# Optimization experiments

Measured on AMD Instinct MI355X. Metric: run time of the kernel, lower is better.

## Reference

```python
import jax, jax.numpy as jnp
import numpy as np

N = 50000      # nodes
F = 256        # num_features
H = 128        # hidden_size
R = 16         # num_relations
E = 800000     # edges
C = 7          # num_classes
NB = 30        # num_bases (hard-coded in module)


def setup_inputs() -> dict:
    key = jax.random.key(0)
    ks = jax.random.split(key, 16)
    g = lambda k, shape, fan_in: jax.random.normal(k, shape, jnp.float32) / np.float32(np.sqrt(fan_in))
    inp = {
        "x": jax.random.normal(ks[0], (N, F), jnp.float32),
        "edge_index": jax.random.randint(ks[1], (2, E), 0, N),
        "edge_norm": jax.random.uniform(ks[2], (E,), jnp.float32),
        "edge_type": jax.random.randint(ks[3], (E,), 0, R),
        "seq_lengths": jax.random.randint(ks[4], (16,), 1, 100),
        "umask": jnp.ones((16, 110), jnp.float32),
        "nodal_attn": 0,
        "avec": 0,
        # RGCNConv (basis decomposition)
        "basis": g(ks[5], (NB, F, H), F),
        "comp": g(ks[6], (R, NB), NB),
        "root1": g(ks[7], (F, H), F),
        "bias1": jnp.zeros((H,), jnp.float32),
        # GraphConv
        "w_rel": g(ks[8], (H, H), H),
        "w_root": g(ks[9], (H, H), H),
        "bias2": jnp.zeros((H,), jnp.float32),
        # classification head
        "lin_w": g(ks[10], (F + H, H), F + H),
        "lin_b": jnp.zeros((H,), jnp.float32),
        "fc_w": g(ks[11], (H, C), H),
        "fc_b": jnp.zeros((C,), jnp.float32),
    }
    return inp


def reference(x, edge_index, edge_norm, edge_type, seq_lengths, umask,
              nodal_attn, avec, basis, comp, root1, bias1,
              w_rel, w_root, bias2, lin_w, lin_b, fc_w, fc_b):
    src, dst = edge_index[0], edge_index[1]

    # ---- RGCNConv: basis-decomposed relational conv, mean aggr per relation ----
    W = jnp.einsum('rb,bio->rio', comp, basis)          # [R,F,H]
    xW = jnp.einsum('ni,rio->nro', x, W)                # [N,R,H]
    msgs = xW[src, edge_type]                           # [E,H]
    seg = dst * R + edge_type                           # (dst, relation) segment id
    cnt = jax.ops.segment_sum(jnp.ones((E,), jnp.float32), seg, num_segments=N * R)
    inv = 1.0 / jnp.maximum(cnt, 1.0)
    agg1 = jax.ops.segment_sum(msgs * inv[seg][:, None], dst, num_segments=N)
    out1 = agg1 + x @ root1 + bias1                     # [N,H]

    # ---- GraphConv: sum aggr + root transform ----
    agg2 = jax.ops.segment_sum(out1[src], dst, num_segments=N)  # [N,H]
    out2 = agg2 @ w_rel + bias2 + out1 @ w_root         # [N,H]

    # ---- classification head (nodal_attn=False path; dropout is identity in eval) ----
    emotions = jnp.concatenate([x, out2], axis=-1)      # [N,F+H]
    hidden = jax.nn.relu(emotions @ lin_w + lin_b)      # [N,H]
    logits = hidden @ fc_w + fc_b                       # [N,C]
    return jax.nn.log_softmax(logits, axis=1)
```

## Files before the change

kernel.cpp:

```cpp
#include <hip/hip_runtime.h>
#include <hip/hip_bf16.h>
#include <stdint.h>

#define NN 50000
#define FF 256
#define HH 128
#define RR 16
#define EE 800000
#define CC 7
#define NB_ 30

typedef __attribute__((ext_vector_type(8))) short short8;
typedef __attribute__((ext_vector_type(4))) float f32x4;

__device__ __forceinline__ float bf2f(unsigned short u){
  union { unsigned int i; float f; } x; x.i = ((unsigned int)u) << 16; return x.f;
}
__device__ __forceinline__ unsigned short f2bf(float f){
  union { unsigned int i; float f; } x; x.f = f;
  unsigned int r = x.i + 0x7fffu + ((x.i >> 16) & 1u);
  return (unsigned short)(r >> 16);
}

__device__ __forceinline__ void gld16(const unsigned short* g, unsigned short* l){
  __builtin_amdgcn_global_load_lds(
      (const __attribute__((address_space(1))) unsigned int*)g,
      (__attribute__((address_space(3))) unsigned int*)l, 16, 0, 0);
}

template<bool BIAS, bool RELU, bool RASTER>
__global__ __launch_bounds__(256) void gemm_bt(
    const unsigned short* __restrict__ A0, int ldA0,
    const unsigned short* __restrict__ A1, int ldA1, int kSplit,
    const unsigned short* __restrict__ Bt,
    unsigned short* __restrict__ Cout, int ldC,
    const float* __restrict__ bias,
    int M, int K)
{
  __shared__ unsigned short Al[128*64];
  __shared__ unsigned short Bl[128*64];
  const int tid  = threadIdx.x;
  const int lane = tid & 63;
  const int wid  = tid >> 6;
  const int wr   = wid >> 1, wc = wid & 1;
  int bm, bn;
  if (RASTER){
    int idx  = blockIdx.x;
    int cidx = (idx & 7)*782 + (idx >> 3);
    int p = cidx >> 7;
    int within = cidx & 127;
    int ph = min(8, 391 - p*8);
    bn = within / ph;
    bm = p*8 + within % ph;
  } else {
    bm = blockIdx.x; bn = blockIdx.y;
  }

  f32x4 acc[4][4];
  #pragma unroll
  for (int m=0;m<4;m++)
    #pragma unroll
    for (int n=0;n<4;n++) acc[m][n] = (f32x4){0.f,0.f,0.f,0.f};

  const int nkt = K >> 6;
  for (int kt=0; kt<nkt; ++kt){
    int c0 = kt*64;
    const unsigned short* Asrc = A0; int lda = ldA0;
    if (c0 >= kSplit){ Asrc = A1; lda = ldA1; c0 -= kSplit; }
    const unsigned short* arow = Asrc + (size_t)(bm*128 + wid*32 + (lane>>3))*lda + c0 + (lane&7)*8;
    const unsigned short* brow = Bt   + (size_t)(bn*128 + wid*32 + (lane>>3))*K  + kt*64 + (lane&7)*8;
    #pragma unroll
    for (int i=0;i<4;i++){
      gld16(arow + (size_t)i*8*lda, &Al[(wid*32 + i*8)*64]);
      gld16(brow + (size_t)i*8*K,   &Bl[(wid*32 + i*8)*64]);
    }
    __syncthreads();
    #pragma unroll
    for (int ks=0; ks<2; ++ks){
      short8 a[4], b[4];
      #pragma unroll
      for (int m=0;m<4;m++)
        a[m] = *(const short8*)&Al[(wr*64 + m*16 + (lane&15))*64 + ks*32 + (lane>>4)*8];
      #pragma unroll
      for (int n=0;n<4;n++)
        b[n] = *(const short8*)&Bl[(wc*64 + n*16 + (lane&15))*64 + ks*32 + (lane>>4)*8];
      #pragma unroll
      for (int m=0;m<4;m++)
        #pragma unroll
        for (int n=0;n<4;n++)
          acc[m][n] = __builtin_amdgcn_mfma_f32_16x16x32_bf16(b[n], a[m], acc[m][n], 0, 0, 0);
    }
    __syncthreads();
  }

  #pragma unroll
  for (int m=0;m<4;m++){
    int row = bm*128 + wr*64 + m*16 + (lane&15);
    if (row < M){
      #pragma unroll
      for (int n=0;n<4;n++){
        int col = bn*128 + wc*64 + n*16 + ((lane>>4)<<2);
        float v0 = acc[m][n][0], v1 = acc[m][n][1], v2 = acc[m][n][2], v3 = acc[m][n][3];
        if (BIAS){ v0 += bias[col]; v1 += bias[col+1]; v2 += bias[col+2]; v3 += bias[col+3]; }
        if (RELU){ v0 = fmaxf(v0,0.f); v1 = fmaxf(v1,0.f); v2 = fmaxf(v2,0.f); v3 = fmaxf(v3,0.f); }
        unsigned int lo = (unsigned int)f2bf(v0) | ((unsigned int)f2bf(v1) << 16);
        unsigned int hi = (unsigned int)f2bf(v2) | ((unsigned int)f2bf(v3) << 16);
        *(uint2*)&Cout[(size_t)row*ldC + col] = make_uint2(lo, hi);
      }
    }
  }
}

__global__ void k_cvt(const float* __restrict__ in, unsigned short* __restrict__ out, int n4){
  int i = blockIdx.x*256 + threadIdx.x;
  if (i >= n4) return;
  float4 v = ((const float4*)in)[i];
  union { unsigned short u[4]; uint2 q; } t;
  t.u[0]=f2bf(v.x); t.u[1]=f2bf(v.y); t.u[2]=f2bf(v.z); t.u[3]=f2bf(v.w);
  ((uint2*)out)[i] = t.q;
}

__global__ __launch_bounds__(256) void k_build_wt(const float* __restrict__ comp,
                                                  const float* __restrict__ basis,
                                                  unsigned short* __restrict__ WT){
  __shared__ float sm[16][129];
  __shared__ float cmp[NB_];
  int r = blockIdx.x >> 4, i0 = (blockIdx.x & 15)*16;
  int o = threadIdx.x & 127, ih = threadIdx.x >> 7;
  if (threadIdx.x < NB_) cmp[threadIdx.x] = comp[r*NB_ + threadIdx.x];
  __syncthreads();
  #pragma unroll
  for (int step=0; step<8; ++step){
    int i = i0 + step*2 + ih;
    float s = 0.f;
    #pragma unroll 6
    for (int b=0;b<NB_;b++) s += cmp[b]*basis[((size_t)b*FF + i)*HH + o];
    sm[step*2+ih][o] = s;
  }
  __syncthreads();
  #pragma unroll
  for (int w=0;w<8;w++){
    int o2 = w*16 + (threadIdx.x>>4);
    int ii = threadIdx.x & 15;
    WT[((size_t)(r*128 + o2))*FF + i0 + ii] = f2bf(sm[ii][o2]);
  }
}

__global__ void k_transpose_cat(const float* __restrict__ in0, int k0,
                                const float* __restrict__ in1, int k1,
                                unsigned short* __restrict__ outT){
  int K = k0 + k1;
  int idx = blockIdx.x*256 + threadIdx.x;
  if (idx >= 128*K) return;
  int o = idx / K, k = idx % K;
  float v = (k < k0) ? in0[(size_t)k*HH + o] : in1[(size_t)(k-k0)*HH + o];
  outT[idx] = f2bf(v);
}

__global__ void k_count(const int* __restrict__ dstv, int* __restrict__ counts){
  int e = blockIdx.x*256 + threadIdx.x;
  if (e >= EE) return;
  atomicAdd(&counts[dstv[e]], 1);
}

__global__ __launch_bounds__(256) void k_scan1(const int* __restrict__ counts,
                                               int* __restrict__ row_ptr,
                                               int* __restrict__ blocksum){
  __shared__ int wsum[4];
  int g = blockIdx.x*256 + threadIdx.x;
  int lane = threadIdx.x & 63, wv = threadIdx.x >> 6;
  int v = (g < NN) ? counts[g] : 0;
  int s = v;
  #pragma unroll
  for (int off=1; off<64; off<<=1){ int t = __shfl_up(s, off, 64); if (lane>=off) s += t; }
  if (lane==63) wsum[wv] = s;
  __syncthreads();
  int wo = 0;
  #pragma unroll
  for (int i=0;i<4;i++) if (i < wv) wo += wsum[i];
  int incl = s + wo;
  if (g < NN) row_ptr[g] = incl - v;
  if (threadIdx.x == 255) blocksum[blockIdx.x] = incl;
}
__global__ __launch_bounds__(256) void k_scan2(int* __restrict__ blocksum, int nb){
  __shared__ int wsum[4];
  int t = threadIdx.x, lane = t & 63, wv = t >> 6;
  int v = (t < nb) ? blocksum[t] : 0;
  int s = v;
  #pragma unroll
  for (int off=1; off<64; off<<=1){ int u = __shfl_up(s, off, 64); if (lane>=off) s += u; }
  if (lane==63) wsum[wv] = s;
  __syncthreads();
  int wo = 0;
  #pragma unroll
  for (int i=0;i<4;i++) if (i < wv) wo += wsum[i];
  if (t < nb) blocksum[t] = s + wo - v;
}
__global__ __launch_bounds__(256) void k_scan3(int* __restrict__ row_ptr,
                                               const int* __restrict__ blocksum){
  int g = blockIdx.x*256 + threadIdx.x;
  if (g < NN) row_ptr[g] += blocksum[blockIdx.x];
  if (g == 0) row_ptr[NN] = EE;
}

__global__ void k_fill(const int* __restrict__ srcv, const int* __restrict__ dstv,
                       const int* __restrict__ etv, const int* __restrict__ row_ptr,
                       int* __restrict__ cursor, int* __restrict__ packed){
  int e = blockIdx.x*256 + threadIdx.x;
  if (e >= EE) return;
  int d = dstv[e];
  int p = atomicAdd(&cursor[d], 1);
  packed[row_ptr[d] + p] = (srcv[e] & 0xffff) | (etv[e] << 16);
}

__global__ __launch_bounds__(256) void k_agg1(const int* __restrict__ row_ptr,
                                              const int* __restrict__ packed,
                                              const unsigned int* __restrict__ xWu,
                                              unsigned int* __restrict__ out1u){
  __shared__ int   cnt[4][RR];
  __shared__ float inv[4][RR];
  const int lane = threadIdx.x & 63;
  const int wv   = threadIdx.x >> 6;
  const int node = blockIdx.x*4 + wv;
  if (lane < RR) cnt[wv][lane] = 0;
  __syncthreads();
  const int b0 = row_ptr[node], b1 = row_ptr[node+1];
  for (int j=b0+lane; j<b1; j+=64) atomicAdd(&cnt[wv][(packed[j]>>16)&15], 1);
  __syncthreads();
  if (lane < RR) inv[wv][lane] = 1.0f / fmaxf((float)cnt[wv][lane], 1.0f);
  __syncthreads();

  float a0=0.f, a1=0.f;
  int j = b0;
  for (; j+8 <= b1; j+=8){
    int pv[8]; unsigned int vv[8];
    #pragma unroll
    for (int q=0;q<8;q++) pv[q] = packed[j+q];
    #pragma unroll
    for (int q=0;q<8;q++)
      vv[q] = xWu[((size_t)(((pv[q]&0xffff)<<4)|((pv[q]>>16)&15)) << 6) + lane];
    #pragma unroll
    for (int q=0;q<8;q++){
      float f = inv[wv][(pv[q]>>16)&15];
      a0 += bf2f((unsigned short)vv[q])*f;
      a1 += bf2f((unsigned short)(vv[q]>>16))*f;
    }
  }
  for (; j+4 <= b1; j+=4){
    int pv[4]; unsigned int vv[4];
    #pragma unroll
    for (int q=0;q<4;q++) pv[q] = packed[j+q];
    #pragma unroll
    for (int q=0;q<4;q++)
      vv[q] = xWu[((size_t)(((pv[q]&0xffff)<<4)|((pv[q]>>16)&15)) << 6) + lane];
    #pragma unroll
    for (int q=0;q<4;q++){
      float f = inv[wv][(pv[q]>>16)&15];
      a0 += bf2f((unsigned short)vv[q])*f;
      a1 += bf2f((unsigned short)(vv[q]>>16))*f;
    }
  }
  for (; j<b1; ++j){
    int p = packed[j];
    unsigned int v = xWu[((size_t)(((p&0xffff)<<4)|((p>>16)&15)) << 6) + lane];
    float f = inv[wv][(p>>16)&15];
    a0 += bf2f((unsigned short)v)*f;
    a1 += bf2f((unsigned short)(v>>16))*f;
  }
  size_t o = (size_t)node*64 + lane;
  unsigned int cur = out1u[o];
  float r0 = bf2f((unsigned short)cur)       + a0;
  float r1 = bf2f((unsigned short)(cur>>16)) + a1;
  out1u[o] = (unsigned int)f2bf(r0) | ((unsigned int)f2bf(r1) << 16);
}

__global__ __launch_bounds__(256) void k_agg2(const int* __restrict__ row_ptr,
                                              const int* __restrict__ packed,
                                              const unsigned int* __restrict__ out1u,
                                              unsigned int* __restrict__ agg2u){
  const int lane = threadIdx.x & 63;
  const int wv   = threadIdx.x >> 6;
  const int node = blockIdx.x*4 + wv;
  const int b0 = row_ptr[node], b1 = row_ptr[node+1];
  float a0=0.f, a1=0.f;
  int j = b0;
  for (; j+8 <= b1; j+=8){
    unsigned int vv[8];
    #pragma unroll
    for (int q=0;q<8;q++)
      vv[q] = out1u[(size_t)(packed[j+q]&0xffff)*64 + lane];
    #pragma unroll
    for (int q=0;q<8;q++){
      a0 += bf2f((unsigned short)vv[q]);
      a1 += bf2f((unsigned short)(vv[q]>>16));
    }
  }
  for (; j+4 <= b1; j+=4){
    unsigned int vv[4];
    #pragma unroll
    for (int q=0;q<4;q++)
      vv[q] = out1u[(size_t)(packed[j+q]&0xffff)*64 + lane];
    #pragma unroll
    for (int q=0;q<4;q++){
      a0 += bf2f((unsigned short)vv[q]);
      a1 += bf2f((unsigned short)(vv[q]>>16));
    }
  }
  for (; j<b1; ++j){
    unsigned int v = out1u[(size_t)(packed[j]&0xffff)*64 + lane];
    a0 += bf2f((unsigned short)v);
    a1 += bf2f((unsigned short)(v>>16));
  }
  agg2u[(size_t)node*64 + lane] = (unsigned int)f2bf(a0) | ((unsigned int)f2bf(a1) << 16);
}

__global__ __launch_bounds__(256) void k_head(const unsigned short* __restrict__ hidden,
                                              const float* __restrict__ fc_w,
                                              const float* __restrict__ fc_b,
                                              float* __restrict__ out){
  int node = blockIdx.x*4 + (threadIdx.x >> 6);
  int lane = threadIdx.x & 63;
  if (node >= NN) return;
  float h0 = bf2f(hidden[(size_t)node*128 + lane*2]);
  float h1 = bf2f(hidden[(size_t)node*128 + lane*2 + 1]);
  float lg[CC];
  #pragma unroll
  for (int c=0;c<CC;c++){
    float p = h0*fc_w[(lane*2)*CC + c] + h1*fc_w[(lane*2+1)*CC + c];
    #pragma unroll
    for (int off=32; off; off>>=1) p += __shfl_down(p, off, 64);
    lg[c] = p;
  }
  if (lane == 0){
    float l[CC]; float m = -1e30f;
    #pragma unroll
    for (int c=0;c<CC;c++){ l[c] = lg[c] + fc_b[c]; m = fmaxf(m, l[c]); }
    float s = 0.f;
    #pragma unroll
    for (int c=0;c<CC;c++) s += expf(l[c]-m);
    float lse = logf(s);
    #pragma unroll
    for (int c=0;c<CC;c++) out[(size_t)node*CC + c] = l[c] - m - lse;
  }
}

extern "C" void kernel_launch(void* const* d_in, const int* in_sizes, int n_in,
                              void* d_out, int out_size, void* d_ws, size_t ws_size,
                              hipStream_t stream)
{
  const float* x      = (const float*)d_in[0];
  const int*   eidx   = (const int*)d_in[1];
  const int*   etype  = (const int*)d_in[3];
  const float* basis  = (const float*)d_in[8];
  const float* comp   = (const float*)d_in[9];
  const float* root1  = (const float*)d_in[10];
  const float* bias1  = (const float*)d_in[11];
  const float* w_rel  = (const float*)d_in[12];
  const float* w_root = (const float*)d_in[13];
  const float* bias2  = (const float*)d_in[14];
  const float* lin_w  = (const float*)d_in[15];
  const float* lin_b  = (const float*)d_in[16];
  const float* fc_w   = (const float*)d_in[17];
  const float* fc_b   = (const float*)d_in[18];
  const int* srcv = eidx;
  const int* dstv = eidx + EE;

  char* w = (char*)d_ws;
  unsigned short* x_bf    = (unsigned short*)(w + 0);
  unsigned short* xW      = (unsigned short*)(w + 25624576);
  unsigned short* hidden  = (unsigned short*)(w + 25624576);
  unsigned short* out2_bf = (unsigned short*)(w + 25624576 + 12812288);
  unsigned short* agg2_bf = (unsigned short*)(w + 25624576 + 25624576);
  unsigned short* WT      = (unsigned short*)(w + 230424576);
  unsigned short* rootT   = (unsigned short*)(w + 231473152);
  unsigned short* W2T     = (unsigned short*)(w + 231538688);
  unsigned short* linT    = (unsigned short*)(w + 231604224);
  unsigned short* out1_bf = (unsigned short*)(w + 231702528);
  int*            counts  = (int*)(w + 244514816);
  int*            row_ptr = (int*)(w + 244715008);
  int*            cursor  = (int*)(w + 244915200);
  int*            packed  = (int*)(w + 245115392);
  int*            blocksum= (int*)(w + 248315392);

  hipMemsetAsync(counts, 0, NN*4, stream);
  hipMemsetAsync(cursor, 0, NN*4, stream);

  k_cvt<<<12500, 256, 0, stream>>>(x, x_bf, NN*FF/4);
  k_build_wt<<<256, 256, 0, stream>>>(comp, basis, WT);
  k_transpose_cat<<<128, 256, 0, stream>>>(root1, 256, nullptr, 0, rootT);
  k_transpose_cat<<<128, 256, 0, stream>>>(w_rel, 128, w_root, 128, W2T);
  k_transpose_cat<<<192, 256, 0, stream>>>(lin_w, 384, nullptr, 0, linT);

  k_count<<<3125, 256, 0, stream>>>(dstv, counts);
  k_scan1<<<196, 256, 0, stream>>>(counts, row_ptr, blocksum);
  k_scan2<<<1, 256, 0, stream>>>(blocksum, 196);
  k_scan3<<<196, 256, 0, stream>>>(row_ptr, blocksum);
  k_fill<<<3125, 256, 0, stream>>>(srcv, dstv, etype, row_ptr, cursor, packed);

  gemm_bt<false,false,true><<<6256, 256, 0, stream>>>(
      x_bf, FF, nullptr, 0, 1<<30, WT, xW, 2048, nullptr, NN, FF);
  {
    dim3 g(391, 1);
    gemm_bt<true,false,false><<<g, 256, 0, stream>>>(
        x_bf, FF, nullptr, 0, 1<<30, rootT, out1_bf, HH, bias1, NN, FF);
  }
  k_agg1<<<12500, 256, 0, stream>>>(row_ptr, packed, (const unsigned int*)xW, (unsigned int*)out1_bf);
  k_agg2<<<12500, 256, 0, stream>>>(row_ptr, packed, (const unsigned int*)out1_bf, (unsigned int*)agg2_bf);
  {
    dim3 g(391, 1);
    gemm_bt<true,false,false><<<g, 256, 0, stream>>>(
        agg2_bf, HH, out1_bf, HH, HH, W2T, out2_bf, HH, bias2, NN, 2*HH);
  }
  {
    dim3 g(391, 1);
    gemm_bt<true,true,false><<<g, 256, 0, stream>>>(
        x_bf, FF, out2_bf, HH, FF, linT, hidden, HH, lin_b, NN, FF+HH);
  }
  k_head<<<12500, 256, 0, stream>>>(hidden, fc_w, fc_b, (float*)d_out);
}
```

Baseline: 408.0 us.

## Fuse xW basis GEMM and root GEMM into one specialized full-K kernel

```diff
diff --git a/kernel.cpp b/kernel.cpp
--- a/kernel.cpp
+++ b/kernel.cpp
@@ -28,7 +28,105 @@
       (__attribute__((address_space(3))) unsigned int*)l, 16, 0, 0);
 }
 
-template<bool BIAS, bool RELU, bool RASTER>
+__global__ __launch_bounds__(256) void k_gemm1(
+    const unsigned short* __restrict__ A,
+    const unsigned short* __restrict__ Bt,
+    unsigned short* __restrict__ xW,
+    unsigned short* __restrict__ out1,
+    const float* __restrict__ bias1)
+{
+  __shared__ unsigned short Al[4][128*64];
+  const int tid  = threadIdx.x;
+  const int lane = tid & 63;
+  const int wid  = tid >> 6;
+  const int wr   = wid >> 1, wc = wid & 1;
+
+  int orig = blockIdx.x;
+  int xcd  = orig & 7, sub = orig >> 3;
+  int cidx = (xcd < 7 ? xcd*831 : 7*831) + sub;
+  int p    = cidx / 136;
+  int wres = cidx - p*136;
+  int ph   = min(8, 391 - p*8);
+  int bn   = wres / ph;
+  int bm   = p*8 + wres % ph;
+
+  {
+    const unsigned short* abase = A + (size_t)(bm*128)*256;
+    int r8 = lane >> 3;
+    int cg = ((lane & 7) ^ r8) * 8;
+    #pragma unroll
+    for (int kt=0; kt<4; ++kt){
+      #pragma unroll
+      for (int i=0;i<4;i++){
+        int rb = wid*32 + i*8;
+        gld16(abase + (size_t)(rb + r8)*256 + kt*64 + cg, &Al[kt][rb*64]);
+      }
+    }
+  }
+
+  short8 breg[4][2][4];
+  {
+    const unsigned short* bbase = Bt + (size_t)(bn*128 + wc*64 + (lane&15))*256 + (lane>>4)*8;
+    #pragma unroll
+    for (int kt=0;kt<4;kt++)
+      #pragma unroll
+      for (int ks=0;ks<2;ks++)
+        #pragma unroll
+        for (int n=0;n<4;n++)
+          breg[kt][ks][n] = *(const short8*)(bbase + (size_t)n*16*256 + kt*64 + ks*32);
+  }
+
+  f32x4 acc[4][4];
+  #pragma unroll
+  for (int m=0;m<4;m++)
+    #pragma unroll
+    for (int n=0;n<4;n++) acc[m][n] = (f32x4){0.f,0.f,0.f,0.f};
+
+  __syncthreads();
+
+  #pragma unroll
+  for (int kt=0;kt<4;kt++){
+    #pragma unroll
+    for (int ks=0;ks<2;ks++){
+      short8 a[4];
+      #pragma unroll
+      for (int m=0;m<4;m++){
+        int row  = wr*64 + m*16 + (lane&15);
+        int slot = ((ks<<2) + (lane>>4)) ^ (lane&7);
+        a[m] = *(const short8*)&Al[kt][row*64 + slot*8];
+      }
+      #pragma unroll
+      for (int m=0;m<4;m++)
+        #pragma unroll
+        for (int n=0;n<4;n++)
+          acc[m][n] = __builtin_amdgcn_mfma_f32_16x16x32_bf16(breg[kt][ks][n], a[m], acc[m][n], 0, 0, 0);
+    }
+  }
+
+  #pragma unroll
+  for (int m=0;m<4;m++){
+    int row = bm*128 + wr*64 + m*16 + (lane&15);
+    if (row < NN){
+      #pragma unroll
+      for (int n=0;n<4;n++){
+        int colr = wc*64 + n*16 + ((lane>>4)<<2);
+        float v0 = acc[m][n][0], v1 = acc[m][n][1], v2 = acc[m][n][2], v3 = acc[m][n][3];
+        if (bn == 16){
+          v0 += bias1[colr]; v1 += bias1[colr+1]; v2 += bias1[colr+2]; v3 += bias1[colr+3];
+          unsigned int lo = (unsigned int)f2bf(v0) | ((unsigned int)f2bf(v1) << 16);
+          unsigned int hi = (unsigned int)f2bf(v2) | ((unsigned int)f2bf(v3) << 16);
+          *(uint2*)&out1[(size_t)row*HH + colr] = make_uint2(lo, hi);
+        } else {
+          unsigned int lo = (unsigned int)f2bf(v0) | ((unsigned int)f2bf(v1) << 16);
+          unsigned int hi = (unsigned int)f2bf(v2) | ((unsigned int)f2bf(v3) << 16);
+          *(uint2*)&xW[(size_t)row*2048 + bn*128 + colr] = make_uint2(lo, hi);
+        }
+      }
+    }
+  }
+}
+
+template<bool BIAS, bool RELU>
 __global__ __launch_bounds__(256) void gemm_bt(
     const unsigned short* __restrict__ A0, int ldA0,
     const unsigned short* __restrict__ A1, int ldA1, int kSplit,
@@ -43,18 +141,7 @@
   const int lane = tid & 63;
   const int wid  = tid >> 6;
   const int wr   = wid >> 1, wc = wid & 1;
-  int bm, bn;
-  if (RASTER){
-    int idx  = blockIdx.x;
-    int cidx = (idx & 7)*782 + (idx >> 3);
-    int p = cidx >> 7;
-    int within = cidx & 127;
-    int ph = min(8, 391 - p*8);
-    bn = within / ph;
-    bm = p*8 + within % ph;
-  } else {
-    bm = blockIdx.x; bn = blockIdx.y;
-  }
+  const int bm   = blockIdx.x, bn = blockIdx.y;
 
   f32x4 acc[4][4];
   #pragma unroll
@@ -381,6 +468,7 @@
   int*            cursor  = (int*)(w + 244915200);
   int*            packed  = (int*)(w + 245115392);
   int*            blocksum= (int*)(w + 248315392);
+  (void)rootT;
 
   hipMemsetAsync(counts, 0, NN*4, stream);
   hipMemsetAsync(cursor, 0, NN*4, stream);
@@ -397,23 +485,17 @@
   k_scan3<<<196, 256, 0, stream>>>(row_ptr, blocksum);
   k_fill<<<3125, 256, 0, stream>>>(srcv, dstv, etype, row_ptr, cursor, packed);
 
-  gemm_bt<false,false,true><<<6256, 256, 0, stream>>>(
-      x_bf, FF, nullptr, 0, 1<<30, WT, xW, 2048, nullptr, NN, FF);
-  {
-    dim3 g(391, 1);
-    gemm_bt<true,false,false><<<g, 256, 0, stream>>>(
-        x_bf, FF, nullptr, 0, 1<<30, rootT, out1_bf, HH, bias1, NN, FF);
-  }
+  k_gemm1<<<6647, 256, 0, stream>>>(x_bf, WT, xW, out1_bf, bias1);
   k_agg1<<<12500, 256, 0, stream>>>(row_ptr, packed, (const unsigned int*)xW, (unsigned int*)out1_bf);
   k_agg2<<<12500, 256, 0, stream>>>(row_ptr, packed, (const unsigned int*)out1_bf, (unsigned int*)agg2_bf);
   {
     dim3 g(391, 1);
-    gemm_bt<true,false,false><<<g, 256, 0, stream>>>(
+    gemm_bt<true,false><<<g, 256, 0, stream>>>(
         agg2_bf, HH, out1_bf, HH, HH, W2T, out2_bf, HH, bias2, NN, 2*HH);
   }
   {
     dim3 g(391, 1);
-    gemm_bt<true,true,false><<<g, 256, 0, stream>>>(
+    gemm_bt<true,true><<<g, 256, 0, stream>>>(
         x_bf, FF, out2_bf, HH, FF, linT, hidden, HH, lin_b, NN, FF+HH);
   }
   k_head<<<12500, 256, 0, stream>>>(hidden, fc_w, fc_b, (float*)d_out);
```

Result: slower. 466.3 us (+14.3%).

## Fuse root GEMM into xW GEMM and double-buffer LDS in gemm kernel

Applied to the files above, without the earlier changes.

```diff
diff --git a/kernel.cpp b/kernel.cpp
--- a/kernel.cpp
+++ b/kernel.cpp
@@ -28,42 +28,40 @@
       (__attribute__((address_space(3))) unsigned int*)l, 16, 0, 0);
 }
 
-template<bool BIAS, bool RELU, bool RASTER>
+template<bool BIAS, bool RELU, bool G1>
 __global__ __launch_bounds__(256) void gemm_bt(
     const unsigned short* __restrict__ A0, int ldA0,
     const unsigned short* __restrict__ A1, int ldA1, int kSplit,
     const unsigned short* __restrict__ Bt,
     unsigned short* __restrict__ Cout, int ldC,
     const float* __restrict__ bias,
-    int M, int K)
+    int M, int K,
+    unsigned short* __restrict__ out1, const float* __restrict__ bias1)
 {
-  __shared__ unsigned short Al[128*64];
-  __shared__ unsigned short Bl[128*64];
+  __shared__ unsigned short Al[2][128*64];
+  __shared__ unsigned short Bl[2][128*64];
   const int tid  = threadIdx.x;
   const int lane = tid & 63;
   const int wid  = tid >> 6;
   const int wr   = wid >> 1, wc = wid & 1;
+
   int bm, bn;
-  if (RASTER){
-    int idx  = blockIdx.x;
-    int cidx = (idx & 7)*782 + (idx >> 3);
-    int p = cidx >> 7;
-    int within = cidx & 127;
-    int ph = min(8, 391 - p*8);
-    bn = within / ph;
-    bm = p*8 + within % ph;
+  if (G1){
+    int orig = blockIdx.x;
+    int xcd  = orig & 7, sub = orig >> 3;
+    int cidx = (xcd < 7 ? xcd*831 : 7*831) + sub;
+    int p    = cidx / 136;
+    int wres = cidx - p*136;
+    int ph   = min(8, 391 - p*8);
+    bn = wres / ph;
+    bm = p*8 + wres % ph;
   } else {
     bm = blockIdx.x; bn = blockIdx.y;
   }
 
-  f32x4 acc[4][4];
-  #pragma unroll
-  for (int m=0;m<4;m++)
-    #pragma unroll
-    for (int n=0;n<4;n++) acc[m][n] = (f32x4){0.f,0.f,0.f,0.f};
-
   const int nkt = K >> 6;
-  for (int kt=0; kt<nkt; ++kt){
+
+  auto STAGE = [&](int kt, int pb){
     int c0 = kt*64;
     const unsigned short* Asrc = A0; int lda = ldA0;
     if (c0 >= kSplit){ Asrc = A1; lda = ldA1; c0 -= kSplit; }
@@ -71,19 +69,32 @@
     const unsigned short* brow = Bt   + (size_t)(bn*128 + wid*32 + (lane>>3))*K  + kt*64 + (lane&7)*8;
     #pragma unroll
     for (int i=0;i<4;i++){
-      gld16(arow + (size_t)i*8*lda, &Al[(wid*32 + i*8)*64]);
-      gld16(brow + (size_t)i*8*K,   &Bl[(wid*32 + i*8)*64]);
-    }
-    __syncthreads();
+      gld16(arow + (size_t)i*8*lda, &Al[pb][(wid*32 + i*8)*64]);
+      gld16(brow + (size_t)i*8*K,   &Bl[pb][(wid*32 + i*8)*64]);
+    }
+  };
+
+  f32x4 acc[4][4];
+  #pragma unroll
+  for (int m=0;m<4;m++)
+    #pragma unroll
+    for (int n=0;n<4;n++) acc[m][n] = (f32x4){0.f,0.f,0.f,0.f};
+
+  STAGE(0, 0);
+  __syncthreads();
+
+  int pb = 0;
+  for (int kt=0; kt<nkt; ++kt){
+    if (kt+1 < nkt) STAGE(kt+1, pb^1);
     #pragma unroll
     for (int ks=0; ks<2; ++ks){
       short8 a[4], b[4];
       #pragma unroll
       for (int m=0;m<4;m++)
-        a[m] = *(const short8*)&Al[(wr*64 + m*16 + (lane&15))*64 + ks*32 + (lane>>4)*8];
+        a[m] = *(const short8*)&Al[pb][(wr*64 + m*16 + (lane&15))*64 + ks*32 + (lane>>4)*8];
       #pragma unroll
       for (int n=0;n<4;n++)
-        b[n] = *(const short8*)&Bl[(wc*64 + n*16 + (lane&15))*64 + ks*32 + (lane>>4)*8];
+        b[n] = *(const short8*)&Bl[pb][(wc*64 + n*16 + (lane&15))*64 + ks*32 + (lane>>4)*8];
       #pragma unroll
       for (int m=0;m<4;m++)
         #pragma unroll
@@ -91,6 +102,7 @@
           acc[m][n] = __builtin_amdgcn_mfma_f32_16x16x32_bf16(b[n], a[m], acc[m][n], 0, 0, 0);
     }
     __syncthreads();
+    pb ^= 1;
   }
 
   #pragma unroll
@@ -99,13 +111,27 @@
     if (row < M){
       #pragma unroll
       for (int n=0;n<4;n++){
-        int col = bn*128 + wc*64 + n*16 + ((lane>>4)<<2);
+        int colr = wc*64 + n*16 + ((lane>>4)<<2);
         float v0 = acc[m][n][0], v1 = acc[m][n][1], v2 = acc[m][n][2], v3 = acc[m][n][3];
-        if (BIAS){ v0 += bias[col]; v1 += bias[col+1]; v2 += bias[col+2]; v3 += bias[col+3]; }
-        if (RELU){ v0 = fmaxf(v0,0.f); v1 = fmaxf(v1,0.f); v2 = fmaxf(v2,0.f); v3 = fmaxf(v3,0.f); }
-        unsigned int lo = (unsigned int)f2bf(v0) | ((unsigned int)f2bf(v1) << 16);
-        unsigned int hi = (unsigned int)f2bf(v2) | ((unsigned int)f2bf(v3) << 16);
-        *(uint2*)&Cout[(size_t)row*ldC + col] = make_uint2(lo, hi);
+        if (G1){
+          if (bn == 16){
+            v0 += bias1[colr]; v1 += bias1[colr+1]; v2 += bias1[colr+2]; v3 += bias1[colr+3];
+            unsigned int lo = (unsigned int)f2bf(v0) | ((unsigned int)f2bf(v1) << 16);
+            unsigned int hi = (unsigned int)f2bf(v2) | ((unsigned int)f2bf(v3) << 16);
+            *(uint2*)&out1[(size_t)row*HH + colr] = make_uint2(lo, hi);
+          } else {
+            unsigned int lo = (unsigned int)f2bf(v0) | ((unsigned int)f2bf(v1) << 16);
+            unsigned int hi = (unsigned int)f2bf(v2) | ((unsigned int)f2bf(v3) << 16);
+            *(uint2*)&Cout[(size_t)row*2048 + bn*128 + colr] = make_uint2(lo, hi);
+          }
+        } else {
+          int col = bn*128 + colr;
+          if (BIAS){ v0 += bias[col]; v1 += bias[col+1]; v2 += bias[col+2]; v3 += bias[col+3]; }
+          if (RELU){ v0 = fmaxf(v0,0.f); v1 = fmaxf(v1,0.f); v2 = fmaxf(v2,0.f); v3 = fmaxf(v3,0.f); }
+          unsigned int lo = (unsigned int)f2bf(v0) | ((unsigned int)f2bf(v1) << 16);
+          unsigned int hi = (unsigned int)f2bf(v2) | ((unsigned int)f2bf(v3) << 16);
+          *(uint2*)&Cout[(size_t)row*ldC + col] = make_uint2(lo, hi);
+        }
       }
     }
   }
@@ -381,6 +407,7 @@
   int*            cursor  = (int*)(w + 244915200);
   int*            packed  = (int*)(w + 245115392);
   int*            blocksum= (int*)(w + 248315392);
+  (void)rootT;
 
   hipMemsetAsync(counts, 0, NN*4, stream);
   hipMemsetAsync(cursor, 0, NN*4, stream);
@@ -397,24 +424,19 @@
   k_scan3<<<196, 256, 0, stream>>>(row_ptr, blocksum);
   k_fill<<<3125, 256, 0, stream>>>(srcv, dstv, etype, row_ptr, cursor, packed);
 
-  gemm_bt<false,false,true><<<6256, 256, 0, stream>>>(
-      x_bf, FF, nullptr, 0, 1<<30, WT, xW, 2048, nullptr, NN, FF);
-  {
-    dim3 g(391, 1);
-    gemm_bt<true,false,false><<<g, 256, 0, stream>>>(
-        x_bf, FF, nullptr, 0, 1<<30, rootT, out1_bf, HH, bias1, NN, FF);
-  }
+  gemm_bt<false,false,true><<<6647, 256, 0, stream>>>(
+      x_bf, FF, nullptr, 0, 1<<30, WT, xW, 2048, nullptr, NN, FF, out1_bf, bias1);
   k_agg1<<<12500, 256, 0, stream>>>(row_ptr, packed, (const unsigned int*)xW, (unsigned int*)out1_bf);
   k_agg2<<<12500, 256, 0, stream>>>(row_ptr, packed, (const unsigned int*)out1_bf, (unsigned int*)agg2_bf);
   {
     dim3 g(391, 1);
     gemm_bt<true,false,false><<<g, 256, 0, stream>>>(
-        agg2_bf, HH, out1_bf, HH, HH, W2T, out2_bf, HH, bias2, NN, 2*HH);
+        agg2_bf, HH, out1_bf, HH, HH, W2T, out2_bf, HH, bias2, NN, 2*HH, nullptr, nullptr);
   }
   {
     dim3 g(391, 1);
     gemm_bt<true,true,false><<<g, 256, 0, stream>>>(
-        x_bf, FF, out2_bf, HH, FF, linT, hidden, HH, lin_b, NN, FF+HH);
+        x_bf, FF, out2_bf, HH, FF, linT, hidden, HH, lin_b, NN, FF+HH, nullptr, nullptr);
   }
   k_head<<<12500, 256, 0, stream>>>(hidden, fc_w, fc_b, (float*)d_out);
 }
```

New measurement: 440.7 us. 1.08x slower.

## Fold GraphConv weights into head linear and fuse GEMMs with classification head

Applied to the files above, without the earlier changes.

```diff
diff --git a/kernel.cpp b/kernel.cpp
--- a/kernel.cpp
+++ b/kernel.cpp
@@ -111,6 +111,138 @@
   }
 }
 
+template<bool FHEAD>
+__global__ __launch_bounds__(256) void gemm_small(
+    const unsigned short* __restrict__ A0, int ldA0, int k0,
+    const unsigned short* __restrict__ A1, int ldA1, int k1,
+    const unsigned short* __restrict__ A2, int ldA2,
+    const unsigned short* __restrict__ Bt,
+    unsigned short* __restrict__ Cout,
+    const float* __restrict__ bias,
+    int M, int K,
+    const float* __restrict__ fc_w, const float* __restrict__ fc_b,
+    float* __restrict__ fout)
+{
+  __shared__ unsigned short smem[(64+128)*64];
+  unsigned short* Al = smem;
+  unsigned short* Bl = smem + 64*64;
+  const int lane = threadIdx.x & 63;
+  const int wid  = threadIdx.x >> 6;
+  const int wr   = wid >> 1, wc = wid & 1;
+  const int bm   = blockIdx.x;
+
+  f32x4 acc[2][4];
+  #pragma unroll
+  for (int m=0;m<2;m++)
+    #pragma unroll
+    for (int n=0;n<4;n++) acc[m][n] = (f32x4){0.f,0.f,0.f,0.f};
+
+  const int nkt = K >> 6;
+  for (int kt=0; kt<nkt; ++kt){
+    int c0 = kt*64;
+    const unsigned short* Asrc; int lda;
+    if (c0 < k0){ Asrc = A0; lda = ldA0; }
+    else if (c0 < k0 + k1){ Asrc = A1; lda = ldA1; c0 -= k0; }
+    else { Asrc = A2; lda = ldA2; c0 -= (k0 + k1); }
+    const unsigned short* arow = Asrc + (size_t)(bm*64 + wid*16 + (lane>>3))*lda + c0 + (lane&7)*8;
+    const unsigned short* brow = Bt + (size_t)(wid*32 + (lane>>3))*K + kt*64 + (lane&7)*8;
+    gld16(arow,                 &Al[(wid*16    )*64]);
+    gld16(arow + (size_t)8*lda, &Al[(wid*16 + 8)*64]);
+    #pragma unroll
+    for (int i=0;i<4;i++)
+      gld16(brow + (size_t)(i*8)*K, &Bl[(wid*32 + i*8)*64]);
+    __syncthreads();
+    #pragma unroll
+    for (int ks=0; ks<2; ++ks){
+      short8 a[2], b[4];
+      #pragma unroll
+      for (int m=0;m<2;m++)
+        a[m] = *(const short8*)&Al[(wr*32 + m*16 + (lane&15))*64 + ks*32 + (lane>>4)*8];
+      #pragma unroll
+      for (int n=0;n<4;n++)
+        b[n] = *(const short8*)&Bl[(wc*64 + n*16 + (lane&15))*64 + ks*32 + (lane>>4)*8];
+      #pragma unroll
+      for (int m=0;m<2;m++)
+        #pragma unroll
+        for (int n=0;n<4;n++)
+          acc[m][n] = __builtin_amdgcn_mfma_f32_16x16x32_bf16(b[n], a[m], acc[m][n], 0, 0, 0);
+    }
+    __syncthreads();
+  }
+
+  if (FHEAD){
+    unsigned int* Hu = (unsigned int*)smem;
+    #pragma unroll
+    for (int m=0;m<2;m++){
+      int row = wr*32 + m*16 + (lane&15);
+      #pragma unroll
+      for (int n=0;n<4;n++){
+        int cbase = wc*64 + n*16 + ((lane>>4)<<2);
+        float v0 = fmaxf(acc[m][n][0] + bias[cbase],   0.f);
+        float v1 = fmaxf(acc[m][n][1] + bias[cbase+1], 0.f);
+        float v2 = fmaxf(acc[m][n][2] + bias[cbase+2], 0.f);
+        float v3 = fmaxf(acc[m][n][3] + bias[cbase+3], 0.f);
+        int cp = (cbase>>1) ^ ((row&7)<<1);
+        Hu[row*64 + cp    ] = (unsigned int)f2bf(v0) | ((unsigned int)f2bf(v1) << 16);
+        Hu[row*64 + cp + 1] = (unsigned int)f2bf(v2) | ((unsigned int)f2bf(v3) << 16);
+      }
+    }
+    __syncthreads();
+    float w0[CC], w1[CC];
+    #pragma unroll
+    for (int c=0;c<CC;c++){
+      w0[c] = fc_w[(lane*2)*CC + c];
+      w1[c] = fc_w[(lane*2+1)*CC + c];
+    }
+    for (int i=0;i<16;i++){
+      int r = wid*16 + i;
+      int node = bm*64 + r;
+      if (node >= NN) break;
+      unsigned int h = Hu[r*64 + (lane ^ ((r&7)<<1))];
+      float h0 = bf2f((unsigned short)h);
+      float h1 = bf2f((unsigned short)(h>>16));
+      float lg[CC];
+      #pragma unroll
+      for (int c=0;c<CC;c++){
+        float p = h0*w0[c] + h1*w1[c];
+        #pragma unroll
+        for (int off=32; off; off>>=1) p += __shfl_down(p, off, 64);
+        lg[c] = p;
+      }
+      if (lane == 0){
+        float l[CC]; float mx = -1e30f;
+        #pragma unroll
+        for (int c=0;c<CC;c++){ l[c] = lg[c] + fc_b[c]; mx = fmaxf(mx, l[c]); }
+        float s = 0.f;
+        #pragma unroll
+        for (int c=0;c<CC;c++) s += expf(l[c]-mx);
+        float lse = logf(s);
+        #pragma unroll
+        for (int c=0;c<CC;c++) fout[(size_t)node*CC + c] = l[c] - mx - lse;
+      }
+    }
+    return;
+  }
+
+  #pragma unroll
+  for (int m=0;m<2;m++){
+    int row = bm*64 + wr*32 + m*16 + (lane&15);
+    if (row < M){
+      #pragma unroll
+      for (int n=0;n<4;n++){
+        int col = wc*64 + n*16 + ((lane>>4)<<2);
+        float v0 = acc[m][n][0] + bias[col];
+        float v1 = acc[m][n][1] + bias[col+1];
+        float v2 = acc[m][n][2] + bias[col+2];
+        float v3 = acc[m][n][3] + bias[col+3];
+        unsigned int lo = (unsigned int)f2bf(v0) | ((unsigned int)f2bf(v1) << 16);
+        unsigned int hi = (unsigned int)f2bf(v2) | ((unsigned int)f2bf(v3) << 16);
+        *(uint2*)&Cout[(size_t)row*HH + col] = make_uint2(lo, hi);
+      }
+    }
+  }
+}
+
 __global__ void k_cvt(const float* __restrict__ in, unsigned short* __restrict__ out, int n4){
   int i = blockIdx.x*256 + threadIdx.x;
   if (i >= n4) return;
@@ -147,14 +279,34 @@
 }
 
 __global__ void k_transpose_cat(const float* __restrict__ in0, int k0,
-                                const float* __restrict__ in1, int k1,
                                 unsigned short* __restrict__ outT){
-  int K = k0 + k1;
   int idx = blockIdx.x*256 + threadIdx.x;
-  if (idx >= 128*K) return;
-  int o = idx / K, k = idx % K;
-  float v = (k < k0) ? in0[(size_t)k*HH + o] : in1[(size_t)(k-k0)*HH + o];
-  outT[idx] = f2bf(v);
+  if (idx >= 128*k0) return;
+  int o = idx / k0, k = idx % k0;
+  outT[idx] = f2bf(in0[(size_t)k*HH + o]);
+}
+
+__global__ __launch_bounds__(256) void k_fuse_w(const float* __restrict__ w_rel,
+                                                const float* __restrict__ w_root,
+                                                const float* __restrict__ lin_w,
+                                                const float* __restrict__ lin_b,
+                                                const float* __restrict__ bias2,
+                                                unsigned short* __restrict__ BtF,
+                                                float* __restrict__ biasF){
+  int o = blockIdx.x;
+  int t = threadIdx.x;
+  BtF[(size_t)o*512 + t] = f2bf(lin_w[(size_t)t*HH + o]);
+  const float* Wsrc = (t < 128) ? w_rel : w_root;
+  int k = t & 127;
+  float s = 0.f;
+  #pragma unroll 4
+  for (int j=0;j<128;j++) s += Wsrc[k*128 + j] * lin_w[(size_t)(256+j)*HH + o];
+  BtF[(size_t)o*512 + 256 + ((t<128)?0:128) + k] = f2bf(s);
+  if (blockIdx.x == 0 && t < 128){
+    float b = lin_b[t];
+    for (int j=0;j<128;j++) b += bias2[j] * lin_w[(size_t)(256+j)*HH + t];
+    biasF[t] = b;
+  }
 }
 
 __global__ void k_count(const int* __restrict__ dstv, int* __restrict__ counts){
@@ -312,36 +464,6 @@
     a1 += bf2f((unsigned short)(v>>16));
   }
   agg2u[(size_t)node*64 + lane] = (unsigned int)f2bf(a0) | ((unsigned int)f2bf(a1) << 16);
-}
-
-__global__ __launch_bounds__(256) void k_head(const unsigned short* __restrict__ hidden,
-                                              const float* __restrict__ fc_w,
-                                              const float* __restrict__ fc_b,
-                                              float* __restrict__ out){
-  int node = blockIdx.x*4 + (threadIdx.x >> 6);
-  int lane = threadIdx.x & 63;
-  if (node >= NN) return;
-  float h0 = bf2f(hidden[(size_t)node*128 + lane*2]);
-  float h1 = bf2f(hidden[(size_t)node*128 + lane*2 + 1]);
-  float lg[CC];
-  #pragma unroll
-  for (int c=0;c<CC;c++){
-    float p = h0*fc_w[(lane*2)*CC + c] + h1*fc_w[(lane*2+1)*CC + c];
-    #pragma unroll
-    for (int off=32; off; off>>=1) p += __shfl_down(p, off, 64);
-    lg[c] = p;
-  }
-  if (lane == 0){
-    float l[CC]; float m = -1e30f;
-    #pragma unroll
-    for (int c=0;c<CC;c++){ l[c] = lg[c] + fc_b[c]; m = fmaxf(m, l[c]); }
-    float s = 0.f;
-    #pragma unroll
-    for (int c=0;c<CC;c++) s += expf(l[c]-m);
-    float lse = logf(s);
-    #pragma unroll
-    for (int c=0;c<CC;c++) out[(size_t)node*CC + c] = l[c] - m - lse;
-  }
 }
 
 extern "C" void kernel_launch(void* const* d_in, const int* in_sizes, int n_in,
@@ -368,13 +490,11 @@
   char* w = (char*)d_ws;
   unsigned short* x_bf    = (unsigned short*)(w + 0);
   unsigned short* xW      = (unsigned short*)(w + 25624576);
-  unsigned short* hidden  = (unsigned short*)(w + 25624576);
-  unsigned short* out2_bf = (unsigned short*)(w + 25624576 + 12812288);
-  unsigned short* agg2_bf = (unsigned short*)(w + 25624576 + 25624576);
+  unsigned short* agg2_bf = (unsigned short*)(w + 25624576 + 12812288);
   unsigned short* WT      = (unsigned short*)(w + 230424576);
   unsigned short* rootT   = (unsigned short*)(w + 231473152);
-  unsigned short* W2T     = (unsigned short*)(w + 231538688);
-  unsigned short* linT    = (unsigned short*)(w + 231604224);
+  unsigned short* BtF     = (unsigned short*)(w + 231538688);
+  float*          biasF   = (float*)         (w + 231669760);
   unsigned short* out1_bf = (unsigned short*)(w + 231702528);
   int*            counts  = (int*)(w + 244514816);
   int*            row_ptr = (int*)(w + 244715008);
@@ -387,9 +507,8 @@
 
   k_cvt<<<12500, 256, 0, stream>>>(x, x_bf, NN*FF/4);
   k_build_wt<<<256, 256, 0, stream>>>(comp, basis, WT);
-  k_transpose_cat<<<128, 256, 0, stream>>>(root1, 256, nullptr, 0, rootT);
-  k_transpose_cat<<<128, 256, 0, stream>>>(w_rel, 128, w_root, 128, W2T);
-  k_transpose_cat<<<192, 256, 0, stream>>>(lin_w, 384, nullptr, 0, linT);
+  k_transpose_cat<<<128, 256, 0, stream>>>(root1, 256, rootT);
+  k_fuse_w<<<128, 256, 0, stream>>>(w_rel, w_root, lin_w, lin_b, bias2, BtF, biasF);
 
   k_count<<<3125, 256, 0, stream>>>(dstv, counts);
   k_scan1<<<196, 256, 0, stream>>>(counts, row_ptr, blocksum);
@@ -399,22 +518,12 @@
 
   gemm_bt<false,false,true><<<6256, 256, 0, stream>>>(
       x_bf, FF, nullptr, 0, 1<<30, WT, xW, 2048, nullptr, NN, FF);
-  {
-    dim3 g(391, 1);
-    gemm_bt<true,false,false><<<g, 256, 0, stream>>>(
-        x_bf, FF, nullptr, 0, 1<<30, rootT, out1_bf, HH, bias1, NN, FF);
-  }
+  gemm_small<false><<<782, 256, 0, stream>>>(
+      x_bf, FF, 1<<30, nullptr, 0, 0, nullptr, 0,
+      rootT, out1_bf, bias1, NN, FF, nullptr, nullptr, nullptr);
   k_agg1<<<12500, 256, 0, stream>>>(row_ptr, packed, (const unsigned int*)xW, (unsigned int*)out1_bf);
   k_agg2<<<12500, 256, 0, stream>>>(row_ptr, packed, (const unsigned int*)out1_bf, (unsigned int*)agg2_bf);
-  {
-    dim3 g(391, 1);
-    gemm_bt<true,false,false><<<g, 256, 0, stream>>>(
-        agg2_bf, HH, out1_bf, HH, HH, W2T, out2_bf, HH, bias2, NN, 2*HH);
-  }
-  {
-    dim3 g(391, 1);
-    gemm_bt<true,true,false><<<g, 256, 0, stream>>>(
-        x_bf, FF, out2_bf, HH, FF, linT, hidden, HH, lin_b, NN, FF+HH);
-  }
-  k_head<<<12500, 256, 0, stream>>>(hidden, fc_w, fc_b, (float*)d_out);
-}
+  gemm_small<true><<<782, 256, 0, stream>>>(
+      x_bf, FF, FF, agg2_bf, HH, HH, out1_bf, HH,
+      BtF, nullptr, biasF, NN, 512, fc_w, fc_b, (float*)d_out);
+}
```

Result: no change. 412.6 us (+1.1%).
